# Optimization experiments

Measured on AMD Instinct MI355X. Metric: run time of the kernel, lower is better.

## Reference

```python
import jax, jax.numpy as jnp
import numpy as np

N_USERS = 4096
N_ITEMS = 8192
N_NODES = N_USERS + N_ITEMS
N_EDGES = 393216
D = 256
N_LAYERS = 3
MAX_TIME = 366
SLOPE = 0.2  # args.slope for LeakyReLU


def setup_inputs() -> dict:
    key = jax.random.key(0)
    ks = jax.random.split(key, 10)
    user_embd = jax.random.normal(ks[0], (N_USERS, D), jnp.float32) * 0.05
    item_embd = jax.random.normal(ks[1], (N_ITEMS, D), jnp.float32) * 0.05
    # interaction-weight parameters are initialized to ones in the original module
    w_p = jnp.ones((N_NODES, N_NODES), jnp.float32)
    w_n = jnp.ones((N_NODES, N_NODES), jnp.float32)
    layer_W = jax.random.normal(ks[2], (N_LAYERS, D, D), jnp.float32) * (1.0 / np.sqrt(D))
    time_table = jax.random.normal(ks[3], (MAX_TIME, D), jnp.float32) * 0.05
    # time-decayed positive/negative adjacency values (exp decay in (0,1])
    val_p = jax.random.uniform(ks[4], (N_EDGES,), jnp.float32)
    val_n = jax.random.uniform(ks[5], (N_EDGES,), jnp.float32)
    src = jax.random.randint(ks[6], (N_EDGES,), 0, N_NODES, dtype=jnp.int32)
    dst = jax.random.randint(ks[7], (N_EDGES,), 0, N_NODES, dtype=jnp.int32)
    time_idx = jax.random.randint(ks[8], (N_EDGES,), 0, MAX_TIME, dtype=jnp.int32)
    return {
        "user_embd": user_embd, "item_embd": item_embd,
        "w_p": w_p, "w_n": w_n, "layer_W": layer_W, "time_table": time_table,
        "val_p": val_p, "val_n": val_n,
        "src": src, "dst": dst, "time_idx": time_idx,
    }


def reference(user_embd, item_embd, w_p, w_n, layer_W, time_table,
              val_p, val_n, src, dst, time_idx):
    # weighted_pos_neg_matix: edge weight = T_p*w_p[src,dst] - T_n*w_n[src,dst]
    edge_w = val_p * w_p[src, dst] - val_n * w_n[src, dst]          # [E]
    # TimeEmbedding lookup per edge
    edge_feat = time_table[time_idx]                                 # [E, D]
    h = jnp.concatenate([user_embd, item_embd], axis=0)              # [N, D]
    embs = [h]  # layer-0 embeddings are kept unnormalized, as in the original
    for i in range(N_LAYERS):
        # GCNLayer: linear transform, weighted message passing over the
        # sparse graph with per-edge time features, LeakyReLU activation
        hw = h @ layer_W[i]                                          # [N, D]
        msg = (hw[src] + edge_feat) * edge_w[:, None]                # [E, D]
        agg = jax.ops.segment_sum(msg, dst, num_segments=N_NODES)   # [N, D]
        h = jax.nn.leaky_relu(agg, SLOPE)
        # F.normalize(p=2, dim=1) on the layer output; next layer consumes
        # the UN-normalized embeddings (matches the torch forward loop)
        norm = jnp.sqrt(jnp.sum(h * h, axis=1, keepdims=True))
        embs.append(h / jnp.maximum(norm, 1e-12))
    node_embedding = jnp.concatenate(embs, axis=1)                   # [N, (L+1)*D]
    # user_embedding = node_embedding[:N_USERS], item = node_embedding[N_USERS:]
    return node_embedding
```

## Files before the change

### kernel.cpp

```cpp
#include <hip/hip_runtime.h>

#define N_USERS  4096
#define N_NODES  12288
#define N_EDGES  393216
#define D        256
#define SLOPE    0.2f
#define PAD      128
#define SENT     0x7FFFFFFF

static __device__ __forceinline__ ushort f2bf_rtne(float f) {
    unsigned int u = __float_as_uint(f);
    u += 0x7FFFu + ((u >> 16) & 1u);
    return (ushort)(u >> 16);
}

__global__ void k_zero_counts(int* __restrict__ counts) {
    int i = blockIdx.x * blockDim.x + threadIdx.x;
    if (i < N_NODES) counts[i] = 0;
}

__global__ void k_scatter_ell(const float* __restrict__ wp, const float* __restrict__ wn,
                              const float* __restrict__ valp, const float* __restrict__ valn,
                              const int* __restrict__ src, const int* __restrict__ dst,
                              const int* __restrict__ tix,
                              int* __restrict__ counts, int2* __restrict__ ell) {
    int e = blockIdx.x * blockDim.x + threadIdx.x;
    if (e >= N_EDGES) return;
    int s = src[e], d0 = dst[e];
    size_t mi = (size_t)s * N_NODES + (size_t)d0;
    float w = valp[e] * wp[mi] - valn[e] * wn[mi];
    int slot = atomicAdd(&counts[d0], 1);
    ell[(size_t)d0 * PAD + slot] = make_int2((s << 16) | (tix[e] << 7) | slot,
                                             __float_as_int(w));
}

#define CE_SHFL(v, pp, kk, ss)                                   \
    {                                                            \
        int ok = __shfl_xor(v.x, ss, 64);                        \
        int ov = __shfl_xor(v.y, ss, 64);                        \
        bool lower = ((lane & (ss)) == 0);                       \
        bool up    = (((pp) & (kk)) == 0);                       \
        bool keep  = ((v.x < ok) == (lower == up));              \
        if (!keep) { v.x = ok; v.y = ov; }                       \
    }

__global__ __launch_bounds__(256) void k_build_B_init(
        const int* __restrict__ counts, int2* __restrict__ ell,
        const float* __restrict__ T,
        const float* __restrict__ user, const float* __restrict__ item,
        float* __restrict__ Bm, float* __restrict__ h, float* __restrict__ out) {
    int wv = threadIdx.x >> 6, lane = threadIdx.x & 63;
    int n = blockIdx.x * 4 + wv;
    int m = counts[n];
    int2* row = &ell[(size_t)n * PAD];

    int2 a = row[lane];
    int2 b = row[lane + 64];
    if (lane >= m)      a = make_int2(SENT, 0);
    if (lane + 64 >= m) b = make_int2(SENT, 0);
#pragma unroll
    for (int k = 2; k <= 128; k <<= 1) {
        if (k == 128) {
            if (a.x > b.x) { int2 t = a; a = b; b = t; }
        }
#pragma unroll
        for (int s = (k == 128 ? 32 : (k >> 1)); s >= 1; s >>= 1) {
            CE_SHFL(a, lane, k, s);
            CE_SHFL(b, lane + 64, k, s);
        }
    }
    row[lane] = a;
    row[lane + 64] = b;

    const float4* T4 = (const float4*)T;
    float4 acc = make_float4(0.f, 0.f, 0.f, 0.f);
    for (int half = 0; half < 2; ++half) {
        int base = half * 64;
        if (m <= base) break;
        int mm = min(64, m - base);
        int2 v = half ? b : a;
        int   te = (v.x >> 7) & 0x1FF;
        float we = __int_as_float(v.y);
        int j = 0;
        for (; j + 4 <= mm; j += 4) {
            int   t0 = __shfl(te, j),     t1 = __shfl(te, j + 1),
                  t2 = __shfl(te, j + 2), t3 = __shfl(te, j + 3);
            float w0 = __shfl(we, j),     w1 = __shfl(we, j + 1),
                  w2 = __shfl(we, j + 2), w3 = __shfl(we, j + 3);
            float4 r0 = T4[t0 * 64 + lane];
            float4 r1 = T4[t1 * 64 + lane];
            float4 r2 = T4[t2 * 64 + lane];
            float4 r3 = T4[t3 * 64 + lane];
            acc.x += w0 * r0.x + w1 * r1.x + w2 * r2.x + w3 * r3.x;
            acc.y += w0 * r0.y + w1 * r1.y + w2 * r2.y + w3 * r3.y;
            acc.z += w0 * r0.z + w1 * r1.z + w2 * r2.z + w3 * r3.z;
            acc.w += w0 * r0.w + w1 * r1.w + w2 * r2.w + w3 * r3.w;
        }
        for (; j < mm; ++j) {
            int t0 = __shfl(te, j); float w0 = __shfl(we, j);
            float4 r0 = T4[t0 * 64 + lane];
            acc.x += w0 * r0.x; acc.y += w0 * r0.y;
            acc.z += w0 * r0.z; acc.w += w0 * r0.w;
        }
    }
    ((float4*)Bm)[n * 64 + lane] = acc;

    const float4* s4 = (n < N_USERS) ? ((const float4*)user) + (size_t)n * 64
                                     : ((const float4*)item) + (size_t)(n - N_USERS) * 64;
    float4 u = s4[lane];
    ((float4*)h)[n * 64 + lane] = u;
    ((float4*)out)[(size_t)n * 256 + lane] = u;
}

__global__ __launch_bounds__(256) void k_gemm(const float* __restrict__ h,
                                              const float* __restrict__ W,
                                              ushort* __restrict__ hwb) {
    __shared__ float As[32 * 64];
    __shared__ float Bs[32 * 64];
    int tid = threadIdx.x;
    int tx = tid & 15, ty = tid >> 4;
    int row0 = blockIdx.x * 64, c0 = blockIdx.y * 64;
    float acc[4][4] = {};
    for (int k0 = 0; k0 < 256; k0 += 32) {
        {
            int r  = tid >> 2;
            int kq = (tid & 3) * 8;
            const float* s = &h[(row0 + r) * 256 + k0 + kq];
            float4 a0 = *(const float4*)s;
            float4 a1 = *(const float4*)(s + 4);
            As[(kq + 0) * 64 + r] = a0.x; As[(kq + 1) * 64 + r] = a0.y;
            As[(kq + 2) * 64 + r] = a0.z; As[(kq + 3) * 64 + r] = a0.w;
            As[(kq + 4) * 64 + r] = a1.x; As[(kq + 5) * 64 + r] = a1.y;
            As[(kq + 6) * 64 + r] = a1.z; As[(kq + 7) * 64 + r] = a1.w;
        }
        {
            int kb = tid >> 3;
            int c8 = (tid & 7) * 8;
            const float* ws = &W[(k0 + kb) * 256 + c0 + c8];
            float4 b0 = *(const float4*)ws;
            float4 b1 = *(const float4*)(ws + 4);
            float* bd = &Bs[kb * 64 + c8];
            bd[0] = b0.x; bd[1] = b0.y; bd[2] = b0.z; bd[3] = b0.w;
            bd[4] = b1.x; bd[5] = b1.y; bd[6] = b1.z; bd[7] = b1.w;
        }
        __syncthreads();
#pragma unroll
        for (int kk = 0; kk < 32; ++kk) {
            float4 a = *(const float4*)&As[kk * 64 + ty * 4];
            float4 b = *(const float4*)&Bs[kk * 64 + tx * 4];
            acc[0][0] += a.x * b.x; acc[0][1] += a.x * b.y; acc[0][2] += a.x * b.z; acc[0][3] += a.x * b.w;
            acc[1][0] += a.y * b.x; acc[1][1] += a.y * b.y; acc[1][2] += a.y * b.z; acc[1][3] += a.y * b.w;
            acc[2][0] += a.z * b.x; acc[2][1] += a.z * b.y; acc[2][2] += a.z * b.z; acc[2][3] += a.z * b.w;
            acc[3][0] += a.w * b.x; acc[3][1] += a.w * b.y; acc[3][2] += a.w * b.z; acc[3][3] += a.w * b.w;
        }
        __syncthreads();
    }
#pragma unroll
    for (int i = 0; i < 4; ++i) {
        ushort4 o;
        o.x = f2bf_rtne(acc[i][0]); o.y = f2bf_rtne(acc[i][1]);
        o.z = f2bf_rtne(acc[i][2]); o.w = f2bf_rtne(acc[i][3]);
        *(ushort4*)&hwb[(size_t)(row0 + ty * 4 + i) * 256 + c0 + tx * 4] = o;
    }
}

#define GATHER4(ACC, W0, RX, RY)                                        \
    ACC.x += (W0) * __int_as_float((int)((RX) << 16));                  \
    ACC.y += (W0) * __int_as_float((int)((RX) & 0xFFFF0000u));          \
    ACC.z += (W0) * __int_as_float((int)((RY) << 16));                  \
    ACC.w += (W0) * __int_as_float((int)((RY) & 0xFFFF0000u));

__global__ __launch_bounds__(256) void k_agg(
        const int* __restrict__ counts, const int2* __restrict__ ell,
        const ushort* __restrict__ hwb, const float* __restrict__ Bm,
        float* __restrict__ h, float* __restrict__ out, int layer) {
    int wv = threadIdx.x >> 6, lane = threadIdx.x & 63;
    int n = blockIdx.x * 4 + wv;
    int m = counts[n];
    const uint2* hw2 = (const uint2*)hwb;
    const int2* row = &ell[(size_t)n * PAD];
    float4 acc = ((const float4*)Bm)[n * 64 + lane];
    for (int base = 0; base < m; base += 64) {
        int idx = base + lane;
        int2 md = (idx < m) ? row[idx] : make_int2(SENT, 0);
        int   se = md.x >> 16;
        float we = __int_as_float(md.y);
        int mm = min(64, m - base);
        int j = 0;
        for (; j + 4 <= mm; j += 4) {
            int   s0 = __shfl(se, j),     s1 = __shfl(se, j + 1),
                  s2 = __shfl(se, j + 2), s3 = __shfl(se, j + 3);
            float w0 = __shfl(we, j),     w1 = __shfl(we, j + 1),
                  w2 = __shfl(we, j + 2), w3 = __shfl(we, j + 3);
            uint2 r0 = hw2[s0 * 64 + lane];
            uint2 r1 = hw2[s1 * 64 + lane];
            uint2 r2 = hw2[s2 * 64 + lane];
            uint2 r3 = hw2[s3 * 64 + lane];
            GATHER4(acc, w0, r0.x, r0.y);
            GATHER4(acc, w1, r1.x, r1.y);
            GATHER4(acc, w2, r2.x, r2.y);
            GATHER4(acc, w3, r3.x, r3.y);
        }
        for (; j < mm; ++j) {
            int s0 = __shfl(se, j); float w0 = __shfl(we, j);
            uint2 r0 = hw2[s0 * 64 + lane];
            GATHER4(acc, w0, r0.x, r0.y);
        }
    }
    float4 v;
    v.x = (acc.x >= 0.f) ? acc.x : SLOPE * acc.x;
    v.y = (acc.y >= 0.f) ? acc.y : SLOPE * acc.y;
    v.z = (acc.z >= 0.f) ? acc.z : SLOPE * acc.z;
    v.w = (acc.w >= 0.f) ? acc.w : SLOPE * acc.w;
    ((float4*)h)[n * 64 + lane] = v;
    float sq = v.x * v.x + v.y * v.y + v.z * v.z + v.w * v.w;
#pragma unroll
    for (int off = 1; off < 64; off <<= 1) sq += __shfl_xor(sq, off, 64);
    float scale = 1.0f / fmaxf(sqrtf(sq), 1e-12f);
    float4 o = make_float4(v.x * scale, v.y * scale, v.z * scale, v.w * scale);
    ((float4*)out)[(size_t)n * 256 + (size_t)(layer + 1) * 64 + lane] = o;
}

extern "C" void kernel_launch(void* const* d_in, const int* in_sizes, int n_in,
                              void* d_out, int out_size, void* d_ws, size_t ws_size,
                              hipStream_t stream) {
    const float* user  = (const float*)d_in[0];
    const float* item  = (const float*)d_in[1];
    const float* wp    = (const float*)d_in[2];
    const float* wn    = (const float*)d_in[3];
    const float* layW  = (const float*)d_in[4];
    const float* ttab  = (const float*)d_in[5];
    const float* valp  = (const float*)d_in[6];
    const float* valn  = (const float*)d_in[7];
    const int*   src   = (const int*)d_in[8];
    const int*   dst   = (const int*)d_in[9];
    const int*   tix   = (const int*)d_in[10];
    float* out = (float*)d_out;

    char* p = (char*)d_ws;
    auto carve = [&](size_t bytes) {
        char* r = p;
        p += (bytes + 255) & ~(size_t)255;
        return r;
    };
    int*    counts = (int*)   carve((size_t)N_NODES * 4);
    int2*   ell    = (int2*)  carve((size_t)N_NODES * PAD * 8);
    float*  Bm     = (float*) carve((size_t)N_NODES * D * 4);
    float*  h      = (float*) carve((size_t)N_NODES * D * 4);
    ushort* hwb    = (ushort*)carve((size_t)N_NODES * D * 2);

    k_zero_counts<<<(N_NODES + 255) / 256, 256, 0, stream>>>(counts);
    k_scatter_ell<<<N_EDGES / 256, 256, 0, stream>>>(wp, wn, valp, valn, src, dst, tix,
                                                     counts, ell);
    k_build_B_init<<<N_NODES / 4, 256, 0, stream>>>(counts, ell, ttab, user, item,
                                                    Bm, h, out);
    for (int l = 0; l < 3; ++l) {
        k_gemm<<<dim3(N_NODES / 64, 4), 256, 0, stream>>>(h, layW + (size_t)l * 256 * 256, hwb);
        k_agg<<<N_NODES / 4, 256, 0, stream>>>(counts, ell, hwb, Bm, h, out, l);
    }
}
```

Before: 1.111 ms.

## Fuse all stages into one cooperative persistent kernel with grid syncs

Replaces the eight separate launches (zero counts, ELL scatter, sort and time-feature build, and three GEMM+aggregate pairs) with one cooperative kernel that loops over work with grid-stride loops and separates phases with grid.sync. This removes per-launch overhead and inter-kernel gaps. In exchange the grid is capped at 384 blocks, so memory-latency-bound phases like the random w_p/w_n gather run with fewer resident waves, and every phase pays a grid barrier.

```diff
diff --git a/kernel.cpp b/kernel.cpp
--- a/kernel.cpp
+++ b/kernel.cpp
@@ -1,4 +1,7 @@
 #include <hip/hip_runtime.h>
+#include <hip/hip_cooperative_groups.h>
+
+namespace cg = cooperative_groups;
 
 #define N_USERS  4096
 #define N_NODES  12288
@@ -7,31 +10,12 @@
 #define SLOPE    0.2f
 #define PAD      128
 #define SENT     0x7FFFFFFF
+#define N_TILES  768
 
 static __device__ __forceinline__ ushort f2bf_rtne(float f) {
     unsigned int u = __float_as_uint(f);
     u += 0x7FFFu + ((u >> 16) & 1u);
     return (ushort)(u >> 16);
-}
-
-__global__ void k_zero_counts(int* __restrict__ counts) {
-    int i = blockIdx.x * blockDim.x + threadIdx.x;
-    if (i < N_NODES) counts[i] = 0;
-}
-
-__global__ void k_scatter_ell(const float* __restrict__ wp, const float* __restrict__ wn,
-                              const float* __restrict__ valp, const float* __restrict__ valn,
-                              const int* __restrict__ src, const int* __restrict__ dst,
-                              const int* __restrict__ tix,
-                              int* __restrict__ counts, int2* __restrict__ ell) {
-    int e = blockIdx.x * blockDim.x + threadIdx.x;
-    if (e >= N_EDGES) return;
-    int s = src[e], d0 = dst[e];
-    size_t mi = (size_t)s * N_NODES + (size_t)d0;
-    float w = valp[e] * wp[mi] - valn[e] * wn[mi];
-    int slot = atomicAdd(&counts[d0], 1);
-    ell[(size_t)d0 * PAD + slot] = make_int2((s << 16) | (tix[e] << 7) | slot,
-                                             __float_as_int(w));
 }
 
 #define CE_SHFL(v, pp, kk, ss)                                   \
@@ -44,181 +28,208 @@
         if (!keep) { v.x = ok; v.y = ov; }                       \
     }
 
-__global__ __launch_bounds__(256) void k_build_B_init(
-        const int* __restrict__ counts, int2* __restrict__ ell,
-        const float* __restrict__ T,
-        const float* __restrict__ user, const float* __restrict__ item,
-        float* __restrict__ Bm, float* __restrict__ h, float* __restrict__ out) {
-    int wv = threadIdx.x >> 6, lane = threadIdx.x & 63;
-    int n = blockIdx.x * 4 + wv;
-    int m = counts[n];
-    int2* row = &ell[(size_t)n * PAD];
-
-    int2 a = row[lane];
-    int2 b = row[lane + 64];
-    if (lane >= m)      a = make_int2(SENT, 0);
-    if (lane + 64 >= m) b = make_int2(SENT, 0);
-#pragma unroll
-    for (int k = 2; k <= 128; k <<= 1) {
-        if (k == 128) {
-            if (a.x > b.x) { int2 t = a; a = b; b = t; }
-        }
-#pragma unroll
-        for (int s = (k == 128 ? 32 : (k >> 1)); s >= 1; s >>= 1) {
-            CE_SHFL(a, lane, k, s);
-            CE_SHFL(b, lane + 64, k, s);
-        }
-    }
-    row[lane] = a;
-    row[lane + 64] = b;
-
-    const float4* T4 = (const float4*)T;
-    float4 acc = make_float4(0.f, 0.f, 0.f, 0.f);
-    for (int half = 0; half < 2; ++half) {
-        int base = half * 64;
-        if (m <= base) break;
-        int mm = min(64, m - base);
-        int2 v = half ? b : a;
-        int   te = (v.x >> 7) & 0x1FF;
-        float we = __int_as_float(v.y);
-        int j = 0;
-        for (; j + 4 <= mm; j += 4) {
-            int   t0 = __shfl(te, j),     t1 = __shfl(te, j + 1),
-                  t2 = __shfl(te, j + 2), t3 = __shfl(te, j + 3);
-            float w0 = __shfl(we, j),     w1 = __shfl(we, j + 1),
-                  w2 = __shfl(we, j + 2), w3 = __shfl(we, j + 3);
-            float4 r0 = T4[t0 * 64 + lane];
-            float4 r1 = T4[t1 * 64 + lane];
-            float4 r2 = T4[t2 * 64 + lane];
-            float4 r3 = T4[t3 * 64 + lane];
-            acc.x += w0 * r0.x + w1 * r1.x + w2 * r2.x + w3 * r3.x;
-            acc.y += w0 * r0.y + w1 * r1.y + w2 * r2.y + w3 * r3.y;
-            acc.z += w0 * r0.z + w1 * r1.z + w2 * r2.z + w3 * r3.z;
-            acc.w += w0 * r0.w + w1 * r1.w + w2 * r2.w + w3 * r3.w;
-        }
-        for (; j < mm; ++j) {
-            int t0 = __shfl(te, j); float w0 = __shfl(we, j);
-            float4 r0 = T4[t0 * 64 + lane];
-            acc.x += w0 * r0.x; acc.y += w0 * r0.y;
-            acc.z += w0 * r0.z; acc.w += w0 * r0.w;
-        }
-    }
-    ((float4*)Bm)[n * 64 + lane] = acc;
-
-    const float4* s4 = (n < N_USERS) ? ((const float4*)user) + (size_t)n * 64
-                                     : ((const float4*)item) + (size_t)(n - N_USERS) * 64;
-    float4 u = s4[lane];
-    ((float4*)h)[n * 64 + lane] = u;
-    ((float4*)out)[(size_t)n * 256 + lane] = u;
-}
-
-__global__ __launch_bounds__(256) void k_gemm(const float* __restrict__ h,
-                                              const float* __restrict__ W,
-                                              ushort* __restrict__ hwb) {
-    __shared__ float As[32 * 64];
-    __shared__ float Bs[32 * 64];
-    int tid = threadIdx.x;
-    int tx = tid & 15, ty = tid >> 4;
-    int row0 = blockIdx.x * 64, c0 = blockIdx.y * 64;
-    float acc[4][4] = {};
-    for (int k0 = 0; k0 < 256; k0 += 32) {
-        {
-            int r  = tid >> 2;
-            int kq = (tid & 3) * 8;
-            const float* s = &h[(row0 + r) * 256 + k0 + kq];
-            float4 a0 = *(const float4*)s;
-            float4 a1 = *(const float4*)(s + 4);
-            As[(kq + 0) * 64 + r] = a0.x; As[(kq + 1) * 64 + r] = a0.y;
-            As[(kq + 2) * 64 + r] = a0.z; As[(kq + 3) * 64 + r] = a0.w;
-            As[(kq + 4) * 64 + r] = a1.x; As[(kq + 5) * 64 + r] = a1.y;
-            As[(kq + 6) * 64 + r] = a1.z; As[(kq + 7) * 64 + r] = a1.w;
-        }
-        {
-            int kb = tid >> 3;
-            int c8 = (tid & 7) * 8;
-            const float* ws = &W[(k0 + kb) * 256 + c0 + c8];
-            float4 b0 = *(const float4*)ws;
-            float4 b1 = *(const float4*)(ws + 4);
-            float* bd = &Bs[kb * 64 + c8];
-            bd[0] = b0.x; bd[1] = b0.y; bd[2] = b0.z; bd[3] = b0.w;
-            bd[4] = b1.x; bd[5] = b1.y; bd[6] = b1.z; bd[7] = b1.w;
-        }
-        __syncthreads();
-#pragma unroll
-        for (int kk = 0; kk < 32; ++kk) {
-            float4 a = *(const float4*)&As[kk * 64 + ty * 4];
-            float4 b = *(const float4*)&Bs[kk * 64 + tx * 4];
-            acc[0][0] += a.x * b.x; acc[0][1] += a.x * b.y; acc[0][2] += a.x * b.z; acc[0][3] += a.x * b.w;
-            acc[1][0] += a.y * b.x; acc[1][1] += a.y * b.y; acc[1][2] += a.y * b.z; acc[1][3] += a.y * b.w;
-            acc[2][0] += a.z * b.x; acc[2][1] += a.z * b.y; acc[2][2] += a.z * b.z; acc[2][3] += a.z * b.w;
-            acc[3][0] += a.w * b.x; acc[3][1] += a.w * b.y; acc[3][2] += a.w * b.z; acc[3][3] += a.w * b.w;
-        }
-        __syncthreads();
-    }
-#pragma unroll
-    for (int i = 0; i < 4; ++i) {
-        ushort4 o;
-        o.x = f2bf_rtne(acc[i][0]); o.y = f2bf_rtne(acc[i][1]);
-        o.z = f2bf_rtne(acc[i][2]); o.w = f2bf_rtne(acc[i][3]);
-        *(ushort4*)&hwb[(size_t)(row0 + ty * 4 + i) * 256 + c0 + tx * 4] = o;
-    }
-}
-
 #define GATHER4(ACC, W0, RX, RY)                                        \
     ACC.x += (W0) * __int_as_float((int)((RX) << 16));                  \
     ACC.y += (W0) * __int_as_float((int)((RX) & 0xFFFF0000u));          \
     ACC.z += (W0) * __int_as_float((int)((RY) << 16));                  \
     ACC.w += (W0) * __int_as_float((int)((RY) & 0xFFFF0000u));
 
-__global__ __launch_bounds__(256) void k_agg(
-        const int* __restrict__ counts, const int2* __restrict__ ell,
-        const ushort* __restrict__ hwb, const float* __restrict__ Bm,
-        float* __restrict__ h, float* __restrict__ out, int layer) {
-    int wv = threadIdx.x >> 6, lane = threadIdx.x & 63;
-    int n = blockIdx.x * 4 + wv;
-    int m = counts[n];
-    const uint2* hw2 = (const uint2*)hwb;
-    const int2* row = &ell[(size_t)n * PAD];
-    float4 acc = ((const float4*)Bm)[n * 64 + lane];
-    for (int base = 0; base < m; base += 64) {
-        int idx = base + lane;
-        int2 md = (idx < m) ? row[idx] : make_int2(SENT, 0);
-        int   se = md.x >> 16;
-        float we = __int_as_float(md.y);
-        int mm = min(64, m - base);
-        int j = 0;
-        for (; j + 4 <= mm; j += 4) {
-            int   s0 = __shfl(se, j),     s1 = __shfl(se, j + 1),
-                  s2 = __shfl(se, j + 2), s3 = __shfl(se, j + 3);
-            float w0 = __shfl(we, j),     w1 = __shfl(we, j + 1),
-                  w2 = __shfl(we, j + 2), w3 = __shfl(we, j + 3);
-            uint2 r0 = hw2[s0 * 64 + lane];
-            uint2 r1 = hw2[s1 * 64 + lane];
-            uint2 r2 = hw2[s2 * 64 + lane];
-            uint2 r3 = hw2[s3 * 64 + lane];
-            GATHER4(acc, w0, r0.x, r0.y);
-            GATHER4(acc, w1, r1.x, r1.y);
-            GATHER4(acc, w2, r2.x, r2.y);
-            GATHER4(acc, w3, r3.x, r3.y);
-        }
-        for (; j < mm; ++j) {
-            int s0 = __shfl(se, j); float w0 = __shfl(we, j);
-            uint2 r0 = hw2[s0 * 64 + lane];
-            GATHER4(acc, w0, r0.x, r0.y);
-        }
-    }
-    float4 v;
-    v.x = (acc.x >= 0.f) ? acc.x : SLOPE * acc.x;
-    v.y = (acc.y >= 0.f) ? acc.y : SLOPE * acc.y;
-    v.z = (acc.z >= 0.f) ? acc.z : SLOPE * acc.z;
-    v.w = (acc.w >= 0.f) ? acc.w : SLOPE * acc.w;
-    ((float4*)h)[n * 64 + lane] = v;
-    float sq = v.x * v.x + v.y * v.y + v.z * v.z + v.w * v.w;
-#pragma unroll
-    for (int off = 1; off < 64; off <<= 1) sq += __shfl_xor(sq, off, 64);
-    float scale = 1.0f / fmaxf(sqrtf(sq), 1e-12f);
-    float4 o = make_float4(v.x * scale, v.y * scale, v.z * scale, v.w * scale);
-    ((float4*)out)[(size_t)n * 256 + (size_t)(layer + 1) * 64 + lane] = o;
+__global__ __launch_bounds__(256, 2) void k_fused(
+        const float* __restrict__ wp,   const float* __restrict__ wn,
+        const float* __restrict__ valp, const float* __restrict__ valn,
+        const int* __restrict__ src,    const int* __restrict__ dst,
+        const int* __restrict__ tix,    const float* __restrict__ T,
+        const float* __restrict__ user, const float* __restrict__ item,
+        const float* __restrict__ layW,
+        int* __restrict__ counts, int2* __restrict__ ell,
+        float* __restrict__ Bm, float* __restrict__ h,
+        ushort* __restrict__ hwb, float* __restrict__ out) {
+    cg::grid_group grid = cg::this_grid();
+    __shared__ float As[32 * 64];
+    __shared__ float Bs[32 * 64];
+
+    const int tid     = threadIdx.x;
+    const int nBlocks = gridDim.x;
+    const int gThreads = nBlocks * 256;
+    const int gWaves   = nBlocks * 4;
+    const int gtid  = blockIdx.x * 256 + tid;
+    const int lane  = tid & 63;
+    const int gwave = blockIdx.x * 4 + (tid >> 6);
+
+    for (int i = gtid; i < N_NODES; i += gThreads) counts[i] = 0;
+    grid.sync();
+
+    for (int e = gtid; e < N_EDGES; e += gThreads) {
+        int s = src[e], d0 = dst[e];
+        size_t mi = (size_t)s * N_NODES + (size_t)d0;
+        float w = valp[e] * wp[mi] - valn[e] * wn[mi];
+        int slot = atomicAdd(&counts[d0], 1);
+        ell[(size_t)d0 * PAD + slot] = make_int2((s << 16) | (tix[e] << 7) | slot,
+                                                 __float_as_int(w));
+    }
+    grid.sync();
+
+    for (int n = gwave; n < N_NODES; n += gWaves) {
+        int m = counts[n];
+        int2* row = &ell[(size_t)n * PAD];
+        int2 a = row[lane];
+        int2 b = row[lane + 64];
+        if (lane >= m)      a = make_int2(SENT, 0);
+        if (lane + 64 >= m) b = make_int2(SENT, 0);
+#pragma unroll
+        for (int k = 2; k <= 128; k <<= 1) {
+            if (k == 128) {
+                if (a.x > b.x) { int2 t = a; a = b; b = t; }
+            }
+#pragma unroll
+            for (int s = (k == 128 ? 32 : (k >> 1)); s >= 1; s >>= 1) {
+                CE_SHFL(a, lane, k, s);
+                CE_SHFL(b, lane + 64, k, s);
+            }
+        }
+        row[lane] = a;
+        row[lane + 64] = b;
+
+        const float4* T4 = (const float4*)T;
+        float4 acc = make_float4(0.f, 0.f, 0.f, 0.f);
+        for (int half = 0; half < 2; ++half) {
+            int base = half * 64;
+            if (m <= base) break;
+            int mm = min(64, m - base);
+            int2 v = half ? b : a;
+            int   te = (v.x >> 7) & 0x1FF;
+            float we = __int_as_float(v.y);
+            int j = 0;
+            for (; j + 4 <= mm; j += 4) {
+                int   t0 = __shfl(te, j),     t1 = __shfl(te, j + 1),
+                      t2 = __shfl(te, j + 2), t3 = __shfl(te, j + 3);
+                float w0 = __shfl(we, j),     w1 = __shfl(we, j + 1),
+                      w2 = __shfl(we, j + 2), w3 = __shfl(we, j + 3);
+                float4 r0 = T4[t0 * 64 + lane];
+                float4 r1 = T4[t1 * 64 + lane];
+                float4 r2 = T4[t2 * 64 + lane];
+                float4 r3 = T4[t3 * 64 + lane];
+                acc.x += w0 * r0.x + w1 * r1.x + w2 * r2.x + w3 * r3.x;
+                acc.y += w0 * r0.y + w1 * r1.y + w2 * r2.y + w3 * r3.y;
+                acc.z += w0 * r0.z + w1 * r1.z + w2 * r2.z + w3 * r3.z;
+                acc.w += w0 * r0.w + w1 * r1.w + w2 * r2.w + w3 * r3.w;
+            }
+            for (; j < mm; ++j) {
+                int t0 = __shfl(te, j); float w0 = __shfl(we, j);
+                float4 r0 = T4[t0 * 64 + lane];
+                acc.x += w0 * r0.x; acc.y += w0 * r0.y;
+                acc.z += w0 * r0.z; acc.w += w0 * r0.w;
+            }
+        }
+        ((float4*)Bm)[n * 64 + lane] = acc;
+
+        const float4* s4 = (n < N_USERS) ? ((const float4*)user) + (size_t)n * 64
+                                         : ((const float4*)item) + (size_t)(n - N_USERS) * 64;
+        float4 u = s4[lane];
+        ((float4*)h)[n * 64 + lane] = u;
+        ((float4*)out)[(size_t)n * 256 + lane] = u;
+    }
+    grid.sync();
+
+    for (int l = 0; l < 3; ++l) {
+        {
+            const float* W = layW + (size_t)l * 256 * 256;
+            int tx = tid & 15, ty = tid >> 4;
+            for (int tile = blockIdx.x; tile < N_TILES; tile += nBlocks) {
+                int row0 = (tile >> 2) * 64, c0 = (tile & 3) * 64;
+                float acc[4][4] = {};
+                for (int k0 = 0; k0 < 256; k0 += 32) {
+                    {
+                        int r  = tid >> 2;
+                        int kq = (tid & 3) * 8;
+                        const float* s = &h[(row0 + r) * 256 + k0 + kq];
+                        float4 a0 = *(const float4*)s;
+                        float4 a1 = *(const float4*)(s + 4);
+                        As[(kq + 0) * 64 + r] = a0.x; As[(kq + 1) * 64 + r] = a0.y;
+                        As[(kq + 2) * 64 + r] = a0.z; As[(kq + 3) * 64 + r] = a0.w;
+                        As[(kq + 4) * 64 + r] = a1.x; As[(kq + 5) * 64 + r] = a1.y;
+                        As[(kq + 6) * 64 + r] = a1.z; As[(kq + 7) * 64 + r] = a1.w;
+                    }
+                    {
+                        int kb = tid >> 3;
+                        int c8 = (tid & 7) * 8;
+                        const float* ws = &W[(k0 + kb) * 256 + c0 + c8];
+                        float4 b0 = *(const float4*)ws;
+                        float4 b1 = *(const float4*)(ws + 4);
+                        float* bd = &Bs[kb * 64 + c8];
+                        bd[0] = b0.x; bd[1] = b0.y; bd[2] = b0.z; bd[3] = b0.w;
+                        bd[4] = b1.x; bd[5] = b1.y; bd[6] = b1.z; bd[7] = b1.w;
+                    }
+                    __syncthreads();
+#pragma unroll
+                    for (int kk = 0; kk < 32; ++kk) {
+                        float4 a = *(const float4*)&As[kk * 64 + ty * 4];
+                        float4 b = *(const float4*)&Bs[kk * 64 + tx * 4];
+                        acc[0][0] += a.x * b.x; acc[0][1] += a.x * b.y; acc[0][2] += a.x * b.z; acc[0][3] += a.x * b.w;
+                        acc[1][0] += a.y * b.x; acc[1][1] += a.y * b.y; acc[1][2] += a.y * b.z; acc[1][3] += a.y * b.w;
+                        acc[2][0] += a.z * b.x; acc[2][1] += a.z * b.y; acc[2][2] += a.z * b.z; acc[2][3] += a.z * b.w;
+                        acc[3][0] += a.w * b.x; acc[3][1] += a.w * b.y; acc[3][2] += a.w * b.z; acc[3][3] += a.w * b.w;
+                    }
+                    __syncthreads();
+                }
+#pragma unroll
+                for (int i = 0; i < 4; ++i) {
+                    ushort4 o;
+                    o.x = f2bf_rtne(acc[i][0]); o.y = f2bf_rtne(acc[i][1]);
+                    o.z = f2bf_rtne(acc[i][2]); o.w = f2bf_rtne(acc[i][3]);
+                    *(ushort4*)&hwb[(size_t)(row0 + ty * 4 + i) * 256 + c0 + tx * 4] = o;
+                }
+            }
+        }
+        grid.sync();
+
+        for (int n = gwave; n < N_NODES; n += gWaves) {
+            int m = counts[n];
+            const uint2* hw2 = (const uint2*)hwb;
+            const int2* row = &ell[(size_t)n * PAD];
+            float4 acc = ((const float4*)Bm)[n * 64 + lane];
+            for (int base = 0; base < m; base += 64) {
+                int idx = base + lane;
+                int2 md = (idx < m) ? row[idx] : make_int2(SENT, 0);
+                int   se = md.x >> 16;
+                float we = __int_as_float(md.y);
+                int mm = min(64, m - base);
+                int j = 0;
+                for (; j + 4 <= mm; j += 4) {
+                    int   s0 = __shfl(se, j),     s1 = __shfl(se, j + 1),
+                          s2 = __shfl(se, j + 2), s3 = __shfl(se, j + 3);
+                    float w0 = __shfl(we, j),     w1 = __shfl(we, j + 1),
+                          w2 = __shfl(we, j + 2), w3 = __shfl(we, j + 3);
+                    uint2 r0 = hw2[s0 * 64 + lane];
+                    uint2 r1 = hw2[s1 * 64 + lane];
+                    uint2 r2 = hw2[s2 * 64 + lane];
+                    uint2 r3 = hw2[s3 * 64 + lane];
+                    GATHER4(acc, w0, r0.x, r0.y);
+                    GATHER4(acc, w1, r1.x, r1.y);
+                    GATHER4(acc, w2, r2.x, r2.y);
+                    GATHER4(acc, w3, r3.x, r3.y);
+                }
+                for (; j < mm; ++j) {
+                    int s0 = __shfl(se, j); float w0 = __shfl(we, j);
+                    uint2 r0 = hw2[s0 * 64 + lane];
+                    GATHER4(acc, w0, r0.x, r0.y);
+                }
+            }
+            float4 v;
+            v.x = (acc.x >= 0.f) ? acc.x : SLOPE * acc.x;
+            v.y = (acc.y >= 0.f) ? acc.y : SLOPE * acc.y;
+            v.z = (acc.z >= 0.f) ? acc.z : SLOPE * acc.z;
+            v.w = (acc.w >= 0.f) ? acc.w : SLOPE * acc.w;
+            ((float4*)h)[n * 64 + lane] = v;
+            float sq = v.x * v.x + v.y * v.y + v.z * v.z + v.w * v.w;
+#pragma unroll
+            for (int off = 1; off < 64; off <<= 1) sq += __shfl_xor(sq, off, 64);
+            float scale = 1.0f / fmaxf(sqrtf(sq), 1e-12f);
+            float4 o = make_float4(v.x * scale, v.y * scale, v.z * scale, v.w * scale);
+            ((float4*)out)[(size_t)n * 256 + (size_t)(l + 1) * 64 + lane] = o;
+        }
+        if (l < 2) grid.sync();
+    }
 }
 
 extern "C" void kernel_launch(void* const* d_in, const int* in_sizes, int n_in,
@@ -249,13 +260,19 @@
     float*  h      = (float*) carve((size_t)N_NODES * D * 4);
     ushort* hwb    = (ushort*)carve((size_t)N_NODES * D * 2);
 
-    k_zero_counts<<<(N_NODES + 255) / 256, 256, 0, stream>>>(counts);
-    k_scatter_ell<<<N_EDGES / 256, 256, 0, stream>>>(wp, wn, valp, valn, src, dst, tix,
-                                                     counts, ell);
-    k_build_B_init<<<N_NODES / 4, 256, 0, stream>>>(counts, ell, ttab, user, item,
-                                                    Bm, h, out);
-    for (int l = 0; l < 3; ++l) {
-        k_gemm<<<dim3(N_NODES / 64, 4), 256, 0, stream>>>(h, layW + (size_t)l * 256 * 256, hwb);
-        k_agg<<<N_NODES / 4, 256, 0, stream>>>(counts, ell, hwb, Bm, h, out, l);
-    }
+    int maxB = 0;
+    hipOccupancyMaxActiveBlocksPerMultiprocessor(&maxB, k_fused, 256, 0);
+    int blocks = maxB * 256;
+    if (blocks > 384) blocks = 384;
+    if (blocks < 64)  blocks = 64;
+
+    void* args[] = {
+        (void*)&wp, (void*)&wn, (void*)&valp, (void*)&valn,
+        (void*)&src, (void*)&dst, (void*)&tix, (void*)&ttab,
+        (void*)&user, (void*)&item, (void*)&layW,
+        (void*)&counts, (void*)&ell, (void*)&Bm, (void*)&h,
+        (void*)&hwb, (void*)&out
+    };
+    hipLaunchCooperativeKernel((const void*)k_fused, dim3(blocks), dim3(256),
+                               args, 0, stream);
 }
```

Result: slower. 1.577 ms (+42.0%).

## Use bf16 MFMA GEMM with pre-transposed weights and bf16 hidden state

Applied to the files above, without the earlier changes.

Replaces the fp32 shared-memory SGEMM with a bf16 MFMA 16x16x32 kernel that reads A and B operands directly from global memory. A prep kernel transposes and converts the layer weights to bf16, and the hidden state h is now stored in bf16 to feed the MFMA and halve its traffic. The scatter kernel also uses nontemporal loads for the dense w_p/w_n gathers. The bf16 hidden state lowers precision of the layer inputs, and the GEMM has no LDS reuse, relying on cache for operand reuse.

```diff
diff --git a/kernel.cpp b/kernel.cpp
--- a/kernel.cpp
+++ b/kernel.cpp
@@ -8,15 +8,23 @@
 #define PAD      128
 #define SENT     0x7FFFFFFF
 
+typedef __attribute__((ext_vector_type(8))) short short8;
+typedef __attribute__((ext_vector_type(4))) float f32x4;
+
 static __device__ __forceinline__ ushort f2bf_rtne(float f) {
     unsigned int u = __float_as_uint(f);
     u += 0x7FFFu + ((u >> 16) & 1u);
     return (ushort)(u >> 16);
 }
 
-__global__ void k_zero_counts(int* __restrict__ counts) {
-    int i = blockIdx.x * blockDim.x + threadIdx.x;
-    if (i < N_NODES) counts[i] = 0;
+__global__ void k_prep(const float* __restrict__ W, ushort* __restrict__ Wt,
+                       int* __restrict__ counts) {
+    int idx = blockIdx.x * 256 + threadIdx.x;
+    if (idx < N_NODES) counts[idx] = 0;
+    int l = idx >> 16;
+    int r = idx & 65535;
+    int n = r >> 8, k = r & 255;
+    Wt[(size_t)l * 65536 + n * 256 + k] = f2bf_rtne(W[(size_t)l * 65536 + k * 256 + n]);
 }
 
 __global__ void k_scatter_ell(const float* __restrict__ wp, const float* __restrict__ wn,
@@ -28,7 +36,9 @@
     if (e >= N_EDGES) return;
     int s = src[e], d0 = dst[e];
     size_t mi = (size_t)s * N_NODES + (size_t)d0;
-    float w = valp[e] * wp[mi] - valn[e] * wn[mi];
+    float a = __builtin_nontemporal_load(wp + mi);
+    float b = __builtin_nontemporal_load(wn + mi);
+    float w = valp[e] * a - valn[e] * b;
     int slot = atomicAdd(&counts[d0], 1);
     ell[(size_t)d0 * PAD + slot] = make_int2((s << 16) | (tix[e] << 7) | slot,
                                              __float_as_int(w));
@@ -48,7 +58,7 @@
         const int* __restrict__ counts, int2* __restrict__ ell,
         const float* __restrict__ T,
         const float* __restrict__ user, const float* __restrict__ item,
-        float* __restrict__ Bm, float* __restrict__ h, float* __restrict__ out) {
+        float* __restrict__ Bm, ushort* __restrict__ hb, float* __restrict__ out) {
     int wv = threadIdx.x >> 6, lane = threadIdx.x & 63;
     int n = blockIdx.x * 4 + wv;
     int m = counts[n];
@@ -108,59 +118,46 @@
     const float4* s4 = (n < N_USERS) ? ((const float4*)user) + (size_t)n * 64
                                      : ((const float4*)item) + (size_t)(n - N_USERS) * 64;
     float4 u = s4[lane];
-    ((float4*)h)[n * 64 + lane] = u;
+    ((ushort4*)hb)[n * 64 + lane] = make_ushort4(f2bf_rtne(u.x), f2bf_rtne(u.y),
+                                                 f2bf_rtne(u.z), f2bf_rtne(u.w));
     ((float4*)out)[(size_t)n * 256 + lane] = u;
 }
 
-__global__ __launch_bounds__(256) void k_gemm(const float* __restrict__ h,
-                                              const float* __restrict__ W,
+__global__ __launch_bounds__(256) void k_gemm(const ushort* __restrict__ hb,
+                                              const ushort* __restrict__ Wt,
                                               ushort* __restrict__ hwb) {
-    __shared__ float As[32 * 64];
-    __shared__ float Bs[32 * 64];
     int tid = threadIdx.x;
-    int tx = tid & 15, ty = tid >> 4;
-    int row0 = blockIdx.x * 64, c0 = blockIdx.y * 64;
-    float acc[4][4] = {};
-    for (int k0 = 0; k0 < 256; k0 += 32) {
-        {
-            int r  = tid >> 2;
-            int kq = (tid & 3) * 8;
-            const float* s = &h[(row0 + r) * 256 + k0 + kq];
-            float4 a0 = *(const float4*)s;
-            float4 a1 = *(const float4*)(s + 4);
-            As[(kq + 0) * 64 + r] = a0.x; As[(kq + 1) * 64 + r] = a0.y;
-            As[(kq + 2) * 64 + r] = a0.z; As[(kq + 3) * 64 + r] = a0.w;
-            As[(kq + 4) * 64 + r] = a1.x; As[(kq + 5) * 64 + r] = a1.y;
-            As[(kq + 6) * 64 + r] = a1.z; As[(kq + 7) * 64 + r] = a1.w;
-        }
-        {
-            int kb = tid >> 3;
-            int c8 = (tid & 7) * 8;
-            const float* ws = &W[(k0 + kb) * 256 + c0 + c8];
-            float4 b0 = *(const float4*)ws;
-            float4 b1 = *(const float4*)(ws + 4);
-            float* bd = &Bs[kb * 64 + c8];
-            bd[0] = b0.x; bd[1] = b0.y; bd[2] = b0.z; bd[3] = b0.w;
-            bd[4] = b1.x; bd[5] = b1.y; bd[6] = b1.z; bd[7] = b1.w;
-        }
-        __syncthreads();
-#pragma unroll
-        for (int kk = 0; kk < 32; ++kk) {
-            float4 a = *(const float4*)&As[kk * 64 + ty * 4];
-            float4 b = *(const float4*)&Bs[kk * 64 + tx * 4];
-            acc[0][0] += a.x * b.x; acc[0][1] += a.x * b.y; acc[0][2] += a.x * b.z; acc[0][3] += a.x * b.w;
-            acc[1][0] += a.y * b.x; acc[1][1] += a.y * b.y; acc[1][2] += a.y * b.z; acc[1][3] += a.y * b.w;
-            acc[2][0] += a.z * b.x; acc[2][1] += a.z * b.y; acc[2][2] += a.z * b.z; acc[2][3] += a.z * b.w;
-            acc[3][0] += a.w * b.x; acc[3][1] += a.w * b.y; acc[3][2] += a.w * b.z; acc[3][3] += a.w * b.w;
-        }
-        __syncthreads();
-    }
-#pragma unroll
-    for (int i = 0; i < 4; ++i) {
-        ushort4 o;
-        o.x = f2bf_rtne(acc[i][0]); o.y = f2bf_rtne(acc[i][1]);
-        o.z = f2bf_rtne(acc[i][2]); o.w = f2bf_rtne(acc[i][3]);
-        *(ushort4*)&hwb[(size_t)(row0 + ty * 4 + i) * 256 + c0 + tx * 4] = o;
+    int wv = tid >> 6, lane = tid & 63;
+    int quad = lane >> 4, l16 = lane & 15;
+    int row0 = blockIdx.x * 64 + wv * 16;
+    int c0 = blockIdx.y * 64;
+
+    const short8* arow = (const short8*)&hb[(size_t)(row0 + l16) * 256];
+    const short8* b0p  = (const short8*)&Wt[(size_t)(c0 +  0 + l16) * 256];
+    const short8* b1p  = (const short8*)&Wt[(size_t)(c0 + 16 + l16) * 256];
+    const short8* b2p  = (const short8*)&Wt[(size_t)(c0 + 32 + l16) * 256];
+    const short8* b3p  = (const short8*)&Wt[(size_t)(c0 + 48 + l16) * 256];
+
+    f32x4 acc0 = {0.f, 0.f, 0.f, 0.f}, acc1 = acc0, acc2 = acc0, acc3 = acc0;
+#pragma unroll
+    for (int k0 = 0; k0 < 32; k0 += 4) {
+        short8 av = arow[k0 + quad];
+        short8 bv0 = b0p[k0 + quad];
+        short8 bv1 = b1p[k0 + quad];
+        short8 bv2 = b2p[k0 + quad];
+        short8 bv3 = b3p[k0 + quad];
+        acc0 = __builtin_amdgcn_mfma_f32_16x16x32_bf16(av, bv0, acc0, 0, 0, 0);
+        acc1 = __builtin_amdgcn_mfma_f32_16x16x32_bf16(av, bv1, acc1, 0, 0, 0);
+        acc2 = __builtin_amdgcn_mfma_f32_16x16x32_bf16(av, bv2, acc2, 0, 0, 0);
+        acc3 = __builtin_amdgcn_mfma_f32_16x16x32_bf16(av, bv3, acc3, 0, 0, 0);
+    }
+#pragma unroll
+    for (int r = 0; r < 4; ++r) {
+        size_t rowoff = (size_t)(row0 + quad * 4 + r) * 256 + c0 + l16;
+        hwb[rowoff +  0] = f2bf_rtne(acc0[r]);
+        hwb[rowoff + 16] = f2bf_rtne(acc1[r]);
+        hwb[rowoff + 32] = f2bf_rtne(acc2[r]);
+        hwb[rowoff + 48] = f2bf_rtne(acc3[r]);
     }
 }
 
@@ -173,7 +170,7 @@
 __global__ __launch_bounds__(256) void k_agg(
         const int* __restrict__ counts, const int2* __restrict__ ell,
         const ushort* __restrict__ hwb, const float* __restrict__ Bm,
-        float* __restrict__ h, float* __restrict__ out, int layer) {
+        ushort* __restrict__ hb, float* __restrict__ out, int layer) {
     int wv = threadIdx.x >> 6, lane = threadIdx.x & 63;
     int n = blockIdx.x * 4 + wv;
     int m = counts[n];
@@ -212,7 +209,8 @@
     v.y = (acc.y >= 0.f) ? acc.y : SLOPE * acc.y;
     v.z = (acc.z >= 0.f) ? acc.z : SLOPE * acc.z;
     v.w = (acc.w >= 0.f) ? acc.w : SLOPE * acc.w;
-    ((float4*)h)[n * 64 + lane] = v;
+    ((ushort4*)hb)[n * 64 + lane] = make_ushort4(f2bf_rtne(v.x), f2bf_rtne(v.y),
+                                                 f2bf_rtne(v.z), f2bf_rtne(v.w));
     float sq = v.x * v.x + v.y * v.y + v.z * v.z + v.w * v.w;
 #pragma unroll
     for (int off = 1; off < 64; off <<= 1) sq += __shfl_xor(sq, off, 64);
@@ -246,16 +244,17 @@
     int*    counts = (int*)   carve((size_t)N_NODES * 4);
     int2*   ell    = (int2*)  carve((size_t)N_NODES * PAD * 8);
     float*  Bm     = (float*) carve((size_t)N_NODES * D * 4);
-    float*  h      = (float*) carve((size_t)N_NODES * D * 4);
+    ushort* hb     = (ushort*)carve((size_t)N_NODES * D * 2);
     ushort* hwb    = (ushort*)carve((size_t)N_NODES * D * 2);
-
-    k_zero_counts<<<(N_NODES + 255) / 256, 256, 0, stream>>>(counts);
+    ushort* Wt     = (ushort*)carve((size_t)3 * 65536 * 2);
+
+    k_prep<<<768, 256, 0, stream>>>(layW, Wt, counts);
     k_scatter_ell<<<N_EDGES / 256, 256, 0, stream>>>(wp, wn, valp, valn, src, dst, tix,
                                                      counts, ell);
     k_build_B_init<<<N_NODES / 4, 256, 0, stream>>>(counts, ell, ttab, user, item,
-                                                    Bm, h, out);
+                                                    Bm, hb, out);
     for (int l = 0; l < 3; ++l) {
-        k_gemm<<<dim3(N_NODES / 64, 4), 256, 0, stream>>>(h, layW + (size_t)l * 256 * 256, hwb);
-        k_agg<<<N_NODES / 4, 256, 0, stream>>>(counts, ell, hwb, Bm, h, out, l);
-    }
-}
+        k_gemm<<<dim3(N_NODES / 64, 4), 256, 0, stream>>>(hb, Wt + (size_t)l * 65536, hwb);
+        k_agg<<<N_NODES / 4, 256, 0, stream>>>(counts, ell, hwb, Bm, hb, out, l);
+    }
+}
```

Measured after the change: 1.074 ms. 3.4% less time.
